# Kernel tuning notes

Hardware: AMD Instinct MI355X
Metric: run time of the kernel (lower is better)

## Reference

```python
import jax, jax.numpy as jnp
import numpy as np

WD, WH, WW = 1, 7, 7
N = WD * WH * WW  # 49 tokens per window
LN_EPS = 1e-5


def _make_rel_coords_table():
    rd = np.arange(-(WD - 1), WD, dtype=np.float32)
    rh = np.arange(-(WH - 1), WH, dtype=np.float32)
    rw = np.arange(-(WW - 1), WW, dtype=np.float32)
    g = np.stack(np.meshgrid(rd, rh, rw, indexing='ij'), axis=-1)  # (2wd-1,2wh-1,2ww-1,3)
    eps = 1e-6
    g = g / (np.array([WD, WH, WW], np.float32) - (1.0 - eps))
    g = g * 8.0
    g = np.sign(g) * np.log2(np.abs(g) + 1.0) / np.log2(8.0)
    return g[None].astype(np.float32)  # (1,2wd-1,2wh-1,2ww-1,3)


def _make_rel_pos_index():
    coords = np.stack(np.meshgrid(np.arange(WD), np.arange(WH), np.arange(WW), indexing='ij'))
    cf = coords.reshape(3, -1)  # (3,N)
    rel = cf[:, :, None] - cf[:, None, :]  # (3,N,N)
    rel = rel.transpose(1, 2, 0).astype(np.int64)
    rel[..., 0] += WD - 1
    rel[..., 1] += WH - 1
    rel[..., 2] += WW - 1
    rel[..., 0] *= (2 * WH - 1) * (2 * WW - 1)
    rel[..., 1] *= 2 * WW - 1
    return rel.sum(-1).astype(np.int32)  # (N,N)


def setup_inputs() -> dict:
    key = jax.random.key(0)
    ks = jax.random.split(key, 8)
    B, D, H, W, C = 4, 8, 56, 56, 256
    nh, hid = 8, 4 * C

    def init_w(k, shape, fan_in):
        return (jax.random.normal(k, shape, jnp.float32) / np.sqrt(fan_in)).astype(jnp.float32)

    inp = {
        'x': jax.random.normal(ks[0], (B, D, H, W, C), jnp.float32),
        'qkv_w': init_w(ks[1], (3 * C, C), C),
        'q_bias': jnp.zeros((C,), jnp.float32),
        'v_bias': jnp.zeros((C,), jnp.float32),
        'logit_scale': jnp.full((nh, 1, 1), np.log(10.0), jnp.float32),
        'cpb_w1': init_w(ks[2], (512, 3), 3),
        'cpb_b1': jnp.zeros((512,), jnp.float32),
        'cpb_w2': init_w(ks[3], (nh, 512), 512),
        'proj_w': init_w(ks[4], (C, C), C),
        'proj_b': jnp.zeros((C,), jnp.float32),
        'norm1_g': jnp.ones((C,), jnp.float32),
        'norm1_b': jnp.zeros((C,), jnp.float32),
        'fc1_w': init_w(ks[5], (hid, C), C),
        'fc1_b': jnp.zeros((hid,), jnp.float32),
        'fc2_w': init_w(ks[6], (C, hid), hid),
        'fc2_b': jnp.zeros((C,), jnp.float32),
        'norm2_g': jnp.ones((C,), jnp.float32),
        'norm2_b': jnp.zeros((C,), jnp.float32),
        'rel_coords_table': jnp.asarray(_make_rel_coords_table()),
        'rel_pos_index': jnp.asarray(_make_rel_pos_index()),
    }
    return inp


def _layernorm(x, g, b):
    mu = jnp.mean(x, axis=-1, keepdims=True)
    var = jnp.mean(jnp.square(x - mu), axis=-1, keepdims=True)
    return (x - mu) * jax.lax.rsqrt(var + LN_EPS) * g + b


def _l2norm(x):
    # F.normalize(dim=-1): x / max(||x||, 1e-12)
    n = jnp.sqrt(jnp.sum(jnp.square(x), axis=-1, keepdims=True))
    return x / jnp.maximum(n, 1e-12)


def _forward(x, qkv_w, q_bias, v_bias, logit_scale, cpb_w1, cpb_b1, cpb_w2,
             proj_w, proj_b, norm1_g, norm1_b, fc1_w, fc1_b, fc2_w, fc2_b,
             norm2_g, norm2_b, rel_coords_table, rel_pos_index):
    B, D, H, W, C = x.shape
    nh = logit_scale.shape[0]
    hd = C // nh

    # ---- window partition: (B,D,H,W,C) -> (B_, N, C)
    xw = x.reshape(B, D // WD, WD, H // WH, WH, W // WW, WW, C)
    xw = xw.transpose(0, 1, 3, 5, 2, 4, 6, 7).reshape(-1, N, C)
    Bw = xw.shape[0]

    # ---- qkv with (q_bias, 0, v_bias)
    qkv_bias = jnp.concatenate([q_bias, jnp.zeros_like(q_bias), v_bias])
    qkv = xw @ qkv_w.T + qkv_bias  # (Bw,N,3C)
    qkv = qkv.reshape(Bw, N, 3, nh, hd).transpose(2, 0, 3, 1, 4)
    q, k, v = qkv[0], qkv[1], qkv[2]  # (Bw,nh,N,hd)

    # ---- cosine attention with clamped learned logit scale
    attn = jnp.einsum('bhnd,bhmd->bhnm', _l2norm(q), _l2norm(k))
    scale = jnp.exp(jnp.minimum(logit_scale, jnp.float32(np.log(100.0))))  # (nh,1,1)
    attn = attn * scale

    # ---- CPB-MLP relative position bias
    t = rel_coords_table.reshape(-1, 3)
    hcpb = jax.nn.relu(t @ cpb_w1.T + cpb_b1)
    table = hcpb @ cpb_w2.T  # (T, nh)
    rpb = table[rel_pos_index.reshape(-1)].reshape(N, N, nh).transpose(2, 0, 1)
    rpb = 16.0 * jax.nn.sigmoid(rpb)
    attn = attn + rpb[None]

    attn = jax.nn.softmax(attn, axis=-1)
    out = jnp.einsum('bhnm,bhmd->bhnd', attn, v)
    out = out.transpose(0, 2, 1, 3).reshape(Bw, N, C)
    out = out @ proj_w.T + proj_b

    # ---- window reverse
    xr = out.reshape(B, D // WD, H // WH, W // WW, WD, WH, WW, C)
    xr = xr.transpose(0, 1, 4, 2, 5, 3, 6, 7).reshape(B, D, H, W, C)

    # ---- Swin-v2 post-norm residuals
    x = x + _layernorm(xr, norm1_g, norm1_b)
    h = jax.nn.gelu(x @ fc1_w.T + fc1_b, approximate=False)
    y = h @ fc2_w.T + fc2_b
    x = x + _layernorm(y, norm2_g, norm2_b)
    return x


def reference(x, qkv_w, q_bias, v_bias, logit_scale, cpb_w1, cpb_b1, cpb_w2,
              proj_w, proj_b, norm1_g, norm1_b, fc1_w, fc1_b, fc2_w, fc2_b,
              norm2_g, norm2_b, rel_coords_table, rel_pos_index):
    return _forward(x, qkv_w, q_bias, v_bias, logit_scale, cpb_w1, cpb_b1, cpb_w2,
                    proj_w, proj_b, norm1_g, norm1_b, fc1_w, fc1_b, fc2_w, fc2_b,
                    norm2_g, norm2_b, rel_coords_table, rel_pos_index)
```

## Files before the change

kernel.cpp:

```cpp
#include <hip/hip_runtime.h>
#include <hip/hip_bf16.h>

typedef __attribute__((ext_vector_type(8))) short short8_t;
typedef __attribute__((ext_vector_type(4))) float f32x4;

__device__ __forceinline__ float bf2f(unsigned short u) {
    return __uint_as_float(((unsigned)u) << 16);
}
__device__ __forceinline__ unsigned short f2bf(float f) {
    __hip_bfloat16 h = __float2bfloat16(f);
    return *reinterpret_cast<unsigned short*>(&h);
}

__device__ __forceinline__ float fast_gelu(float v) {
    float ax = fabsf(v) * 0.70710678118f;
    float t  = __builtin_amdgcn_rcpf(1.f + 0.3275911f * ax);
    float poly = t * (0.254829592f + t * (-0.284496736f + t * (1.421413741f
               + t * (-1.453152027f + t * 1.061405429f))));
    float e  = __expf(-ax * ax);
    float er = 1.f - poly * e;
    float s  = (v >= 0.f) ? er : -er;
    return 0.5f * v * (1.f + s);
}

__device__ __forceinline__ void async16(const unsigned short* g, unsigned short* l) {
    __builtin_amdgcn_global_load_lds(
        (const __attribute__((address_space(1))) unsigned int*)g,
        (__attribute__((address_space(3))) unsigned int*)l,
        16, 0, 0);
}

__device__ __forceinline__ int win_row_to_token(int r) {
    int wb = r / 49, n = r - wb * 49;
    int wq = wb & 7, hb = (wb >> 3) & 7, d = (wb >> 6) & 7, b = wb >> 9;
    int hh = n / 7, ww2 = n - hh * 7;
    return ((b * 8 + d) * 56 + hb * 7 + hh) * 56 + wq * 7 + ww2;
}

__global__ __launch_bounds__(256) void conv_kernel(
    const float* __restrict__ src, unsigned short* __restrict__ dst, int n4)
{
    int stride = gridDim.x * 256;
    for (int i = blockIdx.x * 256 + threadIdx.x; i < n4; i += stride) {
        float4 v = *reinterpret_cast<const float4*>(&src[(size_t)i * 4]);
        short4 o;
        o.x = (short)f2bf(v.x); o.y = (short)f2bf(v.y);
        o.z = (short)f2bf(v.z); o.w = (short)f2bf(v.w);
        *reinterpret_cast<short4*>(&dst[(size_t)i * 4]) = o;
    }
}

__global__ __launch_bounds__(256) void conv4_kernel(
    const float* __restrict__ s0, unsigned short* __restrict__ d0, int n0,
    const float* __restrict__ s1, unsigned short* __restrict__ d1, int n1,
    const float* __restrict__ s2, unsigned short* __restrict__ d2, int n2,
    const float* __restrict__ s3, unsigned short* __restrict__ d3, int n3)
{
    int stride = gridDim.x * 256;
    int total = n0 + n1 + n2 + n3;
    for (int i = blockIdx.x * 256 + threadIdx.x; i < total; i += stride) {
        const float* s; unsigned short* d; int j = i;
        if (j < n0) { s = s0; d = d0; }
        else if ((j -= n0) < n1) { s = s1; d = d1; }
        else if ((j -= n1) < n2) { s = s2; d = d2; }
        else { j -= n2; s = s3; d = d3; }
        float4 v = *reinterpret_cast<const float4*>(&s[(size_t)j * 4]);
        short4 o;
        o.x = (short)f2bf(v.x); o.y = (short)f2bf(v.y);
        o.z = (short)f2bf(v.z); o.w = (short)f2bf(v.w);
        *reinterpret_cast<short4*>(&d[(size_t)j * 4]) = o;
    }
}

__global__ __launch_bounds__(256) void prep_table_kernel(
    const float* __restrict__ w1, const float* __restrict__ b1,
    const float* __restrict__ w2, const float* __restrict__ tabin,
    float* __restrict__ tableg)
{
    const int i = blockIdx.x;
    const int t = threadIdx.x;
    const float c0 = tabin[i * 3], c1 = tabin[i * 3 + 1], c2 = tabin[i * 3 + 2];
    float part[8] = {0.f, 0.f, 0.f, 0.f, 0.f, 0.f, 0.f, 0.f};
    for (int j = t; j < 512; j += 256) {
        float hv = fmaxf(c0 * w1[j * 3] + c1 * w1[j * 3 + 1] + c2 * w1[j * 3 + 2] + b1[j], 0.f);
        #pragma unroll
        for (int h = 0; h < 8; ++h) part[h] += hv * w2[h * 512 + j];
    }
    #pragma unroll
    for (int h = 0; h < 8; ++h) {
        float v = part[h];
        v += __shfl_xor(v, 1);  v += __shfl_xor(v, 2);  v += __shfl_xor(v, 4);
        v += __shfl_xor(v, 8);  v += __shfl_xor(v, 16); v += __shfl_xor(v, 32);
        part[h] = v;
    }
    __shared__ float red[4][8];
    const int wv = t >> 6, lane = t & 63;
    if (lane == 0) {
        #pragma unroll
        for (int h = 0; h < 8; ++h) red[wv][h] = part[h];
    }
    __syncthreads();
    if (t < 8) tableg[i * 8 + t] = red[0][t] + red[1][t] + red[2][t] + red[3][t];
}

__global__ __launch_bounds__(256) void prep_expand_kernel(
    const float* __restrict__ logit_scale,
    const float* __restrict__ qb, const float* __restrict__ vb,
    const int* __restrict__ rpi, const float* __restrict__ tableg,
    float* __restrict__ scales, float* __restrict__ rpbf,
    float* __restrict__ qkvb)
{
    const int stride = gridDim.x * 256;
    const int gt = blockIdx.x * 256 + threadIdx.x;
    if (gt < 8) scales[gt] = expf(fminf(logit_scale[gt], 4.6051702f));
    for (int i = gt; i < 768; i += stride) {
        float o;
        if (i < 256) o = qb[i];
        else if (i < 512) o = 0.f;
        else o = vb[i - 512];
        qkvb[i] = o;
    }
    for (int e = gt; e < 32768; e += stride) {
        int h = e >> 12, rem = e & 4095;
        int mi = rem >> 10, ji = (rem >> 8) & 3;
        int r16 = (rem >> 4) & 15, g4 = (rem >> 2) & 3, r = rem & 3;
        int i = mi * 16 + g4 * 4 + r, j = ji * 16 + r16;
        float val = 0.f;
        if (i < 49 && j < 49) {
            float xv = tableg[rpi[i * 49 + j] * 8 + h];
            val = 16.f / (1.f + expf(-xv));
        }
        rpbf[e] = val;
    }
}

template<int ACT>
__global__ __launch_bounds__(512) void gemm2_kernel(
    const unsigned short* __restrict__ A, const unsigned short* __restrict__ W,
    const float* __restrict__ bias, unsigned short* __restrict__ C,
    int M, int N, int K, int ntn)
{
    __shared__ unsigned short smem[24576];
    const int tid = threadIdx.x;
    const int lane = tid & 63, wv = tid >> 6;
    const int wr = wv >> 2, wc = wv & 3;
    const int nwg = gridDim.x;
    const int virt = (blockIdx.x & 7) * (nwg >> 3) + (blockIdx.x >> 3);
    const int bn = virt % ntn, bm = virt / ntn;
    const size_t arow0 = (size_t)bm * 128;
    const size_t brow0 = (size_t)bn * 256;
    const int r16 = lane & 15, g4 = lane >> 4;
    const int srow_l = lane >> 2;
    const int sgran = (lane & 3) ^ ((srow_l >> 1) & 3);
    f32x4 acc[4][4] = {};

    auto STAGE = [&](int buf, int kt) {
        unsigned short* As = smem + buf * 4096;
        unsigned short* Bs = smem + 8192 + buf * 8192;
        async16(&A[(arow0 + wv * 16 + srow_l) * (size_t)K + kt + sgran * 8],
                &As[(wv * 16) * 32]);
        #pragma unroll
        for (int i = 0; i < 2; ++i) {
            int row0 = wv * 32 + i * 16;
            async16(&W[(brow0 + row0 + srow_l) * (size_t)K + kt + sgran * 8], &Bs[row0 * 32]);
        }
    };
    auto COMPUTE = [&](int buf) {
        unsigned short* As = smem + buf * 4096;
        unsigned short* Bs = smem + 8192 + buf * 8192;
        short8_t af[4], bfr[4];
        const int gsw = g4 ^ ((r16 >> 1) & 3);
        #pragma unroll
        for (int m = 0; m < 4; ++m) {
            int row = wr * 64 + m * 16 + r16;
            af[m] = *reinterpret_cast<const short8_t*>(&As[row * 32 + gsw * 8]);
        }
        #pragma unroll
        for (int n = 0; n < 4; ++n) {
            int row = wc * 64 + n * 16 + r16;
            bfr[n] = *reinterpret_cast<const short8_t*>(&Bs[row * 32 + gsw * 8]);
        }
        #pragma unroll
        for (int m = 0; m < 4; ++m)
            #pragma unroll
            for (int n = 0; n < 4; ++n)
                acc[m][n] = __builtin_amdgcn_mfma_f32_16x16x32_bf16(af[m], bfr[n], acc[m][n], 0, 0, 0);
    };

    const int nk = K >> 5;
    STAGE(0, 0);
    STAGE(1, 32);
    int cur = 0;
    for (int ks = 0; ks < nk - 1; ++ks) {
        asm volatile("s_waitcnt vmcnt(3)" ::: "memory");
        __builtin_amdgcn_sched_barrier(0);
        asm volatile("s_barrier" ::: "memory");
        COMPUTE(cur);
        __builtin_amdgcn_sched_barrier(0);
        asm volatile("s_barrier" ::: "memory");
        if (ks + 2 < nk) STAGE(cur, (ks + 2) << 5);
        cur ^= 1;
    }
    asm volatile("s_waitcnt vmcnt(0)" ::: "memory");
    __builtin_amdgcn_sched_barrier(0);
    asm volatile("s_barrier" ::: "memory");
    COMPUTE(cur);
    __builtin_amdgcn_sched_barrier(0);
    asm volatile("s_barrier" ::: "memory");

    unsigned short* Cs = smem + wv * 2432;
    const int rbase = g4 * 4;
    const int srow = lane >> 3, scol = (lane & 7) * 8;
    const int gcol0 = bn * 256 + wc * 64;
    #pragma unroll
    for (int p = 0; p < 2; ++p) {
        #pragma unroll
        for (int n = 0; n < 4; ++n) {
            float bv = bias[bn * 256 + wc * 64 + n * 16 + r16];
            #pragma unroll
            for (int m2 = 0; m2 < 2; ++m2) {
                int m = p * 2 + m2;
                #pragma unroll
                for (int r = 0; r < 4; ++r) {
                    float v = acc[m][n][r] + bv;
                    if (ACT == 1) v = fast_gelu(v);
                    Cs[(m2 * 16 + rbase + r) * 76 + n * 16 + r16] = f2bf(v);
                }
            }
        }
        #pragma unroll
        for (int rr = 0; rr < 4; ++rr) {
            int lr = rr * 8 + srow;
            int grow = bm * 128 + wr * 64 + p * 32 + lr;
            short8_t vv = *reinterpret_cast<const short8_t*>(&Cs[lr * 76 + scol]);
            *reinterpret_cast<short8_t*>(&C[(size_t)grow * N + gcol0 + scol]) = vv;
        }
    }
}

template<int SCATTER, int OUT_F32>
__global__ __launch_bounds__(512) void gemm_ln_kernel(
    const unsigned short* __restrict__ A, const unsigned short* __restrict__ W,
    const float* __restrict__ bias, const unsigned short* __restrict__ resid,
    const float* __restrict__ gamma, const float* __restrict__ beta,
    void* __restrict__ Cv, int M, int K)
{
    __shared__ unsigned short smem[24576];
    const int tid = threadIdx.x;
    const int lane = tid & 63, wv = tid >> 6;
    const int wr = wv >> 2, wc = wv & 3;
    const int nwg = gridDim.x;
    const int bm = (blockIdx.x & 7) * (nwg >> 3) + (blockIdx.x >> 3);
    const size_t arow0 = (size_t)bm * 128;
    const int r16 = lane & 15, g4 = lane >> 4;
    const int srow_l = lane >> 2;
    const int sgran = (lane & 3) ^ ((srow_l >> 1) & 3);
    f32x4 acc[4][4] = {};

    auto STAGE = [&](int buf, int kt) {
        unsigned short* As = smem + buf * 4096;
        unsigned short* Bs = smem + 8192 + buf * 8192;
        async16(&A[(arow0 + wv * 16 + srow_l) * (size_t)K + kt + sgran * 8],
                &As[(wv * 16) * 32]);
        #pragma unroll
        for (int i = 0; i < 2; ++i) {
            int row0 = wv * 32 + i * 16;
            async16(&W[(size_t)(row0 + srow_l) * K + kt + sgran * 8], &Bs[row0 * 32]);
        }
    };
    auto COMPUTE = [&](int buf) {
        unsigned short* As = smem + buf * 4096;
        unsigned short* Bs = smem + 8192 + buf * 8192;
        short8_t af[4], bfr[4];
        const int gsw = g4 ^ ((r16 >> 1) & 3);
        #pragma unroll
        for (int m = 0; m < 4; ++m) {
            int row = wr * 64 + m * 16 + r16;
            af[m] = *reinterpret_cast<const short8_t*>(&As[row * 32 + gsw * 8]);
        }
        #pragma unroll
        for (int n = 0; n < 4; ++n) {
            int row = wc * 64 + n * 16 + r16;
            bfr[n] = *reinterpret_cast<const short8_t*>(&Bs[row * 32 + gsw * 8]);
        }
        #pragma unroll
        for (int m = 0; m < 4; ++m)
            #pragma unroll
            for (int n = 0; n < 4; ++n)
                acc[m][n] = __builtin_amdgcn_mfma_f32_16x16x32_bf16(af[m], bfr[n], acc[m][n], 0, 0, 0);
    };

    const int nk = K >> 5;
    STAGE(0, 0);
    STAGE(1, 32);
    int cur = 0;
    for (int ks = 0; ks < nk - 1; ++ks) {
        asm volatile("s_waitcnt vmcnt(3)" ::: "memory");
        __builtin_amdgcn_sched_barrier(0);
        asm volatile("s_barrier" ::: "memory");
        COMPUTE(cur);
        __builtin_amdgcn_sched_barrier(0);
        asm volatile("s_barrier" ::: "memory");
        if (ks + 2 < nk) STAGE(cur, (ks + 2) << 5);
        cur ^= 1;
    }
    asm volatile("s_waitcnt vmcnt(0)" ::: "memory");
    __builtin_amdgcn_sched_barrier(0);
    asm volatile("s_barrier" ::: "memory");
    COMPUTE(cur);
    __builtin_amdgcn_sched_barrier(0);
    asm volatile("s_barrier" ::: "memory");

    float bv[4];
    #pragma unroll
    for (int n = 0; n < 4; ++n) bv[n] = bias[wc * 64 + n * 16 + r16];
    float* psum  = reinterpret_cast<float*>(smem + 19456);
    float* psq   = psum + 512;
    float* stats = psq + 512;
    #pragma unroll
    for (int m = 0; m < 4; ++m) {
        #pragma unroll
        for (int r = 0; r < 4; ++r) {
            float s = 0.f, s2 = 0.f;
            #pragma unroll
            for (int n = 0; n < 4; ++n) {
                float v = acc[m][n][r] + bv[n];
                s += v; s2 += v * v;
            }
            s  += __shfl_xor(s, 1);  s  += __shfl_xor(s, 2);
            s  += __shfl_xor(s, 4);  s  += __shfl_xor(s, 8);
            s2 += __shfl_xor(s2, 1); s2 += __shfl_xor(s2, 2);
            s2 += __shfl_xor(s2, 4); s2 += __shfl_xor(s2, 8);
            if (r16 == 0) {
                int row = wr * 64 + m * 16 + g4 * 4 + r;
                psum[row * 4 + wc] = s;
                psq[row * 4 + wc]  = s2;
            }
        }
    }
    __syncthreads();
    if (tid < 128) {
        f32x4 a = *reinterpret_cast<const f32x4*>(&psum[tid * 4]);
        f32x4 b = *reinterpret_cast<const f32x4*>(&psq[tid * 4]);
        float mu  = (a[0] + a[1] + a[2] + a[3]) * 0.00390625f;
        float ex2 = (b[0] + b[1] + b[2] + b[3]) * 0.00390625f;
        stats[tid * 2]     = mu;
        stats[tid * 2 + 1] = rsqrtf(ex2 - mu * mu + 1e-5f);
    }
    __syncthreads();

    unsigned short* Cs = smem + wv * 2432;
    const int rbase = g4 * 4;
    const int srow = lane >> 3, scol = (lane & 7) * 8;
    const int gcol0 = wc * 64;
    f32x4 gm0 = *reinterpret_cast<const f32x4*>(&gamma[gcol0 + scol]);
    f32x4 gm1 = *reinterpret_cast<const f32x4*>(&gamma[gcol0 + scol + 4]);
    f32x4 bt0 = *reinterpret_cast<const f32x4*>(&beta[gcol0 + scol]);
    f32x4 bt1 = *reinterpret_cast<const f32x4*>(&beta[gcol0 + scol + 4]);
    #pragma unroll
    for (int p = 0; p < 2; ++p) {
        #pragma unroll
        for (int n = 0; n < 4; ++n)
            #pragma unroll
            for (int m2 = 0; m2 < 2; ++m2)
                #pragma unroll
                for (int r = 0; r < 4; ++r)
                    Cs[(m2 * 16 + rbase + r) * 76 + n * 16 + r16] =
                        f2bf(acc[p * 2 + m2][n][r] + bv[n]);
        #pragma unroll
        for (int rr = 0; rr < 4; ++rr) {
            int lr = rr * 8 + srow;
            int lrow = wr * 64 + p * 32 + lr;
            int grow = bm * 128 + lrow;
            size_t orow = SCATTER ? (size_t)win_row_to_token(grow) : (size_t)grow;
            float mu  = stats[lrow * 2];
            float inv = stats[lrow * 2 + 1];
            short8_t cv = *reinterpret_cast<const short8_t*>(&Cs[lr * 76 + scol]);
            short8_t rv = *reinterpret_cast<const short8_t*>(&resid[orow * 256 + gcol0 + scol]);
            float o[8];
            #pragma unroll
            for (int e = 0; e < 8; ++e) {
                float g = (e < 4) ? gm0[e] : gm1[e - 4];
                float bb = (e < 4) ? bt0[e] : bt1[e - 4];
                o[e] = bf2f((unsigned short)rv[e])
                     + (bf2f((unsigned short)cv[e]) - mu) * inv * g + bb;
            }
            if (OUT_F32) {
                float* outp = (float*)Cv + orow * 256 + gcol0 + scol;
                f32x4 o0, o1;
                #pragma unroll
                for (int e = 0; e < 4; ++e) { o0[e] = o[e]; o1[e] = o[e + 4]; }
                *reinterpret_cast<f32x4*>(outp)     = o0;
                *reinterpret_cast<f32x4*>(outp + 4) = o1;
            } else {
                unsigned short* outp = (unsigned short*)Cv + orow * 256 + gcol0 + scol;
                short8_t ov;
                #pragma unroll
                for (int e = 0; e < 8; ++e) ov[e] = (short)f2bf(o[e]);
                *reinterpret_cast<short8_t*>(outp) = ov;
            }
        }
    }
}

__global__ __launch_bounds__(64) void attn_kernel(
    const unsigned short* __restrict__ qkv, const float* __restrict__ scales,
    const float* __restrict__ rpbf, unsigned short* __restrict__ out)
{
    constexpr int QO = 0;
    constexpr int KO = 2560;
    constexpr int VO = 5120;
    constexpr int PO = 0;
    __shared__ unsigned short lds[7424];

    const int blk = blockIdx.x;
    const int h = blk & 7, wb = blk >> 3;
    const int lane = threadIdx.x;
    const int r16 = lane & 15, g4 = lane >> 4;

    const int wq = wb & 7, hb = (wb >> 3) & 7, dd = (wb >> 6) & 7, bb2 = wb >> 9;
    const int tok_base = ((bb2 * 8 + dd) * 56 + hb * 7) * 56 + wq * 7;
    const float sc = scales[h];

    {
        short8_t z = {};
        int d = lane >> 1, j0 = 48 + (lane & 1) * 8;
        *reinterpret_cast<short8_t*>(&lds[VO + d * 72 + j0]) = z;
    }
    #pragma unroll
    for (int sel = 0; sel < 2; ++sel) {
        for (int c = lane; c < 196; c += 64) {
            int row = c >> 2, gi = c & 3;
            int tok = tok_base + (row / 7) * 56 + (row % 7);
            const unsigned short* gp = qkv + (size_t)tok * 768 + sel * 256 + h * 32 + gi * 8;
            short8_t raw = *reinterpret_cast<const short8_t*>(gp);
            float f[8]; float ss = 0.f;
            #pragma unroll
            for (int e = 0; e < 8; ++e) { f[e] = bf2f((unsigned short)raw[e]); ss += f[e] * f[e]; }
            ss += __shfl_xor(ss, 1); ss += __shfl_xor(ss, 2);
            float inv = 1.f / fmaxf(sqrtf(ss), 1e-12f);
            if (sel == 0) inv *= sc;
            short8_t o;
            #pragma unroll
            for (int e = 0; e < 8; ++e) o[e] = (short)f2bf(f[e] * inv);
            *reinterpret_cast<short8_t*>(&lds[(sel ? KO : QO) + row * 40 + gi * 8]) = o;
        }
    }
    for (int c = lane; c < 196; c += 64) {
        int j = c >> 2, gi = c & 3;
        int tok = tok_base + (j / 7) * 56 + (j % 7);
        short8_t raw = *reinterpret_cast<const short8_t*>(
            qkv + (size_t)tok * 768 + 512 + h * 32 + gi * 8);
        #pragma unroll
        for (int e = 0; e < 8; ++e)
            lds[VO + (gi * 8 + e) * 72 + j] = (unsigned short)raw[e];
    }
    __syncthreads();

    short8_t qf[4], kf[4];
    #pragma unroll
    for (int mi = 0; mi < 4; ++mi)
        qf[mi] = *reinterpret_cast<const short8_t*>(&lds[QO + (mi * 16 + r16) * 40 + g4 * 8]);
    #pragma unroll
    for (int ji = 0; ji < 4; ++ji)
        kf[ji] = *reinterpret_cast<const short8_t*>(&lds[KO + (ji * 16 + r16) * 40 + g4 * 8]);
    f32x4 acc[4][4] = {};
    #pragma unroll
    for (int mi = 0; mi < 4; ++mi)
        #pragma unroll
        for (int ji = 0; ji < 4; ++ji)
            acc[mi][ji] = __builtin_amdgcn_mfma_f32_16x16x32_bf16(qf[mi], kf[ji], acc[mi][ji], 0, 0, 0);
    __syncthreads();

    const float* rbf = rpbf + h * 4096 + r16 * 16 + g4 * 4;
    f32x4 rbv[4][4];
    #pragma unroll
    for (int mi = 0; mi < 4; ++mi)
        #pragma unroll
        for (int ji = 0; ji < 4; ++ji)
            rbv[mi][ji] = *reinterpret_cast<const f32x4*>(&rbf[(mi * 4 + ji) * 256]);

    #pragma unroll
    for (int mi = 0; mi < 4; ++mi) {
        #pragma unroll
        for (int r = 0; r < 4; ++r) {
            int i = mi * 16 + g4 * 4 + r;
            float s[4]; float m = -1e30f;
            #pragma unroll
            for (int ji = 0; ji < 4; ++ji) {
                int j = ji * 16 + r16;
                float v = acc[mi][ji][r] + rbv[mi][ji][r];
                s[ji] = (j < 49) ? v : -1e30f;
                m = fmaxf(m, s[ji]);
            }
            m = fmaxf(m, __shfl_xor(m, 1)); m = fmaxf(m, __shfl_xor(m, 2));
            m = fmaxf(m, __shfl_xor(m, 4)); m = fmaxf(m, __shfl_xor(m, 8));
            float p[4]; float sum = 0.f;
            #pragma unroll
            for (int ji = 0; ji < 4; ++ji) {
                p[ji] = (s[ji] > -1e29f) ? __expf(s[ji] - m) : 0.f;
                sum += p[ji];
            }
            sum += __shfl_xor(sum, 1); sum += __shfl_xor(sum, 2);
            sum += __shfl_xor(sum, 4); sum += __shfl_xor(sum, 8);
            float rinv = 1.f / sum;
            #pragma unroll
            for (int ji = 0; ji < 4; ++ji) {
                int j = ji * 16 + r16;
                lds[PO + i * 72 + j] = f2bf(p[ji] * rinv);
            }
        }
    }
    __syncthreads();

    f32x4 acc2[4][2] = {};
    #pragma unroll
    for (int ks = 0; ks < 2; ++ks) {
        short8_t pf[4], vf[2];
        int ko = ks * 32 + g4 * 8;
        #pragma unroll
        for (int mi = 0; mi < 4; ++mi)
            pf[mi] = *reinterpret_cast<const short8_t*>(&lds[PO + (mi * 16 + r16) * 72 + ko]);
        #pragma unroll
        for (int ni = 0; ni < 2; ++ni)
            vf[ni] = *reinterpret_cast<const short8_t*>(&lds[VO + (ni * 16 + r16) * 72 + ko]);
        #pragma unroll
        for (int mi = 0; mi < 4; ++mi)
            #pragma unroll
            for (int ni = 0; ni < 2; ++ni)
                acc2[mi][ni] = __builtin_amdgcn_mfma_f32_16x16x32_bf16(pf[mi], vf[ni], acc2[mi][ni], 0, 0, 0);
    }

    #pragma unroll
    for (int mi = 0; mi < 4; ++mi)
        #pragma unroll
        for (int r = 0; r < 4; ++r) {
            int i = mi * 16 + g4 * 4 + r;
            if (i < 49) {
                size_t ob = (size_t)(wb * 49 + i) * 256 + h * 32;
                out[ob + r16]      = f2bf(acc2[mi][0][r]);
                out[ob + 16 + r16] = f2bf(acc2[mi][1][r]);
            }
        }
}

extern "C" void kernel_launch(void* const* d_in, const int* in_sizes, int n_in,
                              void* d_out, int out_size, void* d_ws, size_t ws_size,
                              hipStream_t stream) {
    const float* x      = (const float*)d_in[0];
    const float* qkv_w  = (const float*)d_in[1];
    const float* q_bias = (const float*)d_in[2];
    const float* v_bias = (const float*)d_in[3];
    const float* lscale = (const float*)d_in[4];
    const float* cpb_w1 = (const float*)d_in[5];
    const float* cpb_b1 = (const float*)d_in[6];
    const float* cpb_w2 = (const float*)d_in[7];
    const float* proj_w = (const float*)d_in[8];
    const float* proj_b = (const float*)d_in[9];
    const float* n1g    = (const float*)d_in[10];
    const float* n1b    = (const float*)d_in[11];
    const float* fc1_w  = (const float*)d_in[12];
    const float* fc1_b  = (const float*)d_in[13];
    const float* fc2_w  = (const float*)d_in[14];
    const float* fc2_b  = (const float*)d_in[15];
    const float* n2g    = (const float*)d_in[16];
    const float* n2b    = (const float*)d_in[17];
    const float* rct    = (const float*)d_in[18];
    const int*   rpi    = (const int*)d_in[19];

    char* ws = (char*)d_ws;
    unsigned short* qkv    = (unsigned short*)(ws);
    unsigned short* hbuf   = (unsigned short*)(ws);
    unsigned short* attn_o = (unsigned short*)(ws + 154140672);
    unsigned short* xb     = (unsigned short*)(ws + 205520896);
    unsigned short* x1     = (unsigned short*)(ws + 205520896);
    unsigned short* wqkv   = (unsigned short*)(ws + 308281344);
    unsigned short* wproj  = (unsigned short*)(ws + 308674560);
    unsigned short* wfc1   = (unsigned short*)(ws + 308805632);
    unsigned short* wfc2   = (unsigned short*)(ws + 309329920);
    float*          rpbf   = (float*)(ws + 309854208);
    float*          scales = (float*)(ws + 310378496);
    float*          qkvb   = (float*)(ws + 310378528);
    float*          tableg = (float*)(ws + 310381600);

    const int M = 100352;

    conv_kernel<<<2048, 256, 0, stream>>>(x, xb, 25690112 / 4);
    conv4_kernel<<<768, 256, 0, stream>>>(qkv_w, wqkv, 49152,
                                          proj_w, wproj, 16384,
                                          fc1_w, wfc1, 65536,
                                          fc2_w, wfc2, 65536);
    prep_table_kernel<<<169, 256, 0, stream>>>(cpb_w1, cpb_b1, cpb_w2, rct, tableg);
    prep_expand_kernel<<<128, 256, 0, stream>>>(lscale, q_bias, v_bias, rpi, tableg,
                                                scales, rpbf, qkvb);
    gemm2_kernel<0><<<2352, 512, 0, stream>>>(xb, wqkv, qkvb, qkv, M, 768, 256, 3);
    attn_kernel<<<16384, 64, 0, stream>>>(qkv, scales, rpbf, attn_o);
    gemm_ln_kernel<1, 0><<<784, 512, 0, stream>>>(attn_o, wproj, proj_b, xb, n1g, n1b,
                                                  x1, M, 256);
    gemm2_kernel<1><<<3136, 512, 0, stream>>>(x1, wfc1, fc1_b, hbuf, M, 1024, 256, 4);
    gemm_ln_kernel<0, 1><<<784, 512, 0, stream>>>(hbuf, wfc2, fc2_b, x1, n2g, n2b,
                                                  d_out, M, 1024);
}
```

Before: 456.9 us.

## Use triple-buffered LDS ring in GEMM kernels to drop per-step barrier

Both the plain GEMM and the GEMM+LayerNorm kernels move from a two-slot LDS double buffer to a three-slot ring. This lets the next stage be issued before compute and removes the second s_barrier in each k-step. The cost is 72KB of LDS per block instead of 48KB, which may lower the number of resident blocks per CU.

```diff
diff --git a/kernel.cpp b/kernel.cpp
--- a/kernel.cpp
+++ b/kernel.cpp
@@ -140,7 +140,7 @@
     const float* __restrict__ bias, unsigned short* __restrict__ C,
     int M, int N, int K, int ntn)
 {
-    __shared__ unsigned short smem[24576];
+    __shared__ unsigned short smem[36864];
     const int tid = threadIdx.x;
     const int lane = tid & 63, wv = tid >> 6;
     const int wr = wv >> 2, wc = wv & 3;
@@ -155,8 +155,8 @@
     f32x4 acc[4][4] = {};
 
     auto STAGE = [&](int buf, int kt) {
-        unsigned short* As = smem + buf * 4096;
-        unsigned short* Bs = smem + 8192 + buf * 8192;
+        unsigned short* As = smem + buf * 12288;
+        unsigned short* Bs = As + 4096;
         async16(&A[(arow0 + wv * 16 + srow_l) * (size_t)K + kt + sgran * 8],
                 &As[(wv * 16) * 32]);
         #pragma unroll
@@ -166,8 +166,8 @@
         }
     };
     auto COMPUTE = [&](int buf) {
-        unsigned short* As = smem + buf * 4096;
-        unsigned short* Bs = smem + 8192 + buf * 8192;
+        unsigned short* As = smem + buf * 12288;
+        unsigned short* Bs = As + 4096;
         short8_t af[4], bfr[4];
         const int gsw = g4 ^ ((r16 >> 1) & 3);
         #pragma unroll
@@ -190,21 +190,20 @@
     const int nk = K >> 5;
     STAGE(0, 0);
     STAGE(1, 32);
-    int cur = 0;
-    for (int ks = 0; ks < nk - 1; ++ks) {
-        asm volatile("s_waitcnt vmcnt(3)" ::: "memory");
+    int cb = 0;
+    for (int ks = 0; ks < nk; ++ks) {
+        if (ks == nk - 1) { asm volatile("s_waitcnt vmcnt(0)" ::: "memory"); }
+        else              { asm volatile("s_waitcnt vmcnt(3)" ::: "memory"); }
         __builtin_amdgcn_sched_barrier(0);
         asm volatile("s_barrier" ::: "memory");
-        COMPUTE(cur);
+        if (ks + 2 < nk) {
+            int sb = cb + 2; if (sb >= 3) sb -= 3;
+            STAGE(sb, (ks + 2) << 5);
+        }
         __builtin_amdgcn_sched_barrier(0);
-        asm volatile("s_barrier" ::: "memory");
-        if (ks + 2 < nk) STAGE(cur, (ks + 2) << 5);
-        cur ^= 1;
-    }
-    asm volatile("s_waitcnt vmcnt(0)" ::: "memory");
-    __builtin_amdgcn_sched_barrier(0);
-    asm volatile("s_barrier" ::: "memory");
-    COMPUTE(cur);
+        COMPUTE(cb);
+        cb = (cb == 2) ? 0 : cb + 1;
+    }
     __builtin_amdgcn_sched_barrier(0);
     asm volatile("s_barrier" ::: "memory");
 
@@ -245,7 +244,7 @@
     const float* __restrict__ gamma, const float* __restrict__ beta,
     void* __restrict__ Cv, int M, int K)
 {
-    __shared__ unsigned short smem[24576];
+    __shared__ unsigned short smem[36864];
     const int tid = threadIdx.x;
     const int lane = tid & 63, wv = tid >> 6;
     const int wr = wv >> 2, wc = wv & 3;
@@ -258,8 +257,8 @@
     f32x4 acc[4][4] = {};
 
     auto STAGE = [&](int buf, int kt) {
-        unsigned short* As = smem + buf * 4096;
-        unsigned short* Bs = smem + 8192 + buf * 8192;
+        unsigned short* As = smem + buf * 12288;
+        unsigned short* Bs = As + 4096;
         async16(&A[(arow0 + wv * 16 + srow_l) * (size_t)K + kt + sgran * 8],
                 &As[(wv * 16) * 32]);
         #pragma unroll
@@ -269,8 +268,8 @@
         }
     };
     auto COMPUTE = [&](int buf) {
-        unsigned short* As = smem + buf * 4096;
-        unsigned short* Bs = smem + 8192 + buf * 8192;
+        unsigned short* As = smem + buf * 12288;
+        unsigned short* Bs = As + 4096;
         short8_t af[4], bfr[4];
         const int gsw = g4 ^ ((r16 >> 1) & 3);
         #pragma unroll
@@ -293,21 +292,20 @@
     const int nk = K >> 5;
     STAGE(0, 0);
     STAGE(1, 32);
-    int cur = 0;
-    for (int ks = 0; ks < nk - 1; ++ks) {
-        asm volatile("s_waitcnt vmcnt(3)" ::: "memory");
+    int cb = 0;
+    for (int ks = 0; ks < nk; ++ks) {
+        if (ks == nk - 1) { asm volatile("s_waitcnt vmcnt(0)" ::: "memory"); }
+        else              { asm volatile("s_waitcnt vmcnt(3)" ::: "memory"); }
         __builtin_amdgcn_sched_barrier(0);
         asm volatile("s_barrier" ::: "memory");
-        COMPUTE(cur);
+        if (ks + 2 < nk) {
+            int sb = cb + 2; if (sb >= 3) sb -= 3;
+            STAGE(sb, (ks + 2) << 5);
+        }
         __builtin_amdgcn_sched_barrier(0);
-        asm volatile("s_barrier" ::: "memory");
-        if (ks + 2 < nk) STAGE(cur, (ks + 2) << 5);
-        cur ^= 1;
-    }
-    asm volatile("s_waitcnt vmcnt(0)" ::: "memory");
-    __builtin_amdgcn_sched_barrier(0);
-    asm volatile("s_barrier" ::: "memory");
-    COMPUTE(cur);
+        COMPUTE(cb);
+        cb = (cb == 2) ? 0 : cb + 1;
+    }
     __builtin_amdgcn_sched_barrier(0);
     asm volatile("s_barrier" ::: "memory");
 
```

Measured after the change: 450.7 us. About the same (-1.4%).
